# Kernel tuning notes

Measured on AMD Instinct MI355X. Metric: run time of the kernel, lower is better.

The kernel has to match this reference:

```python
import jax, jax.numpy as jnp
import numpy as np

D_MODEL = 1024
NUM_HEADS = 16
D_K = D_MODEL // NUM_HEADS
ROPE_THETA = 10000.0


def _rope(x, positions):
    # x: [B, H, S, Dk]; positions: [S] int. Interleaved-pair RoPE, theta=10000.
    half = D_K // 2
    inv_freq = 1.0 / (ROPE_THETA ** (jnp.arange(half, dtype=jnp.float32) * 2.0 / D_K))
    ang = positions.astype(jnp.float32)[:, None] * inv_freq[None, :]  # [S, half]
    cos = jnp.cos(ang)[None, None]  # [1,1,S,half]
    sin = jnp.sin(ang)[None, None]
    x_even = x[..., 0::2]
    x_odd = x[..., 1::2]
    r_even = x_even * cos - x_odd * sin
    r_odd = x_even * sin + x_odd * cos
    out = jnp.stack([r_even, r_odd], axis=-1)  # [B,H,S,half,2]
    return out.reshape(x.shape)


def setup_inputs() -> dict:
    key = jax.random.key(0)
    ks = jax.random.split(key, 5)
    B, S = 4, 2048
    std = (2.0 / (D_MODEL + D_MODEL)) ** 0.5
    return {
        "x": jax.random.normal(ks[0], (B, S, D_MODEL), dtype=jnp.float32),
        "Wq": jax.random.normal(ks[1], (D_MODEL, D_MODEL), dtype=jnp.float32) * std,
        "Wk": jax.random.normal(ks[2], (D_MODEL, D_MODEL), dtype=jnp.float32) * std,
        "Wv": jax.random.normal(ks[3], (D_MODEL, D_MODEL), dtype=jnp.float32) * std,
        "Wo": jax.random.normal(ks[4], (D_MODEL, D_MODEL), dtype=jnp.float32) * std,
        "token_positions": jnp.arange(S, dtype=jnp.int32),
    }


def reference(x, Wq, Wk, Wv, Wo, token_positions):
    B, S, _ = x.shape
    # QKV projections (weights stored [out, in], y = x @ W^T)
    def proj(W):
        y = jnp.einsum('bsi,oi->bso', x, W)
        return y.reshape(B, S, NUM_HEADS, D_K).transpose(0, 2, 1, 3)  # [B,H,S,Dk]
    q = _rope(proj(Wq), token_positions)
    k = _rope(proj(Wk), token_positions)
    v = proj(Wv)
    scores = jnp.einsum('bhqd,bhkd->bhqk', q, k) / jnp.sqrt(jnp.float32(D_K))
    causal = token_positions[:, None] >= token_positions[None, :]  # [S,S]
    scores = jnp.where(causal[None, None], scores, jnp.float32(-1e9))
    probs = jax.nn.softmax(scores, axis=-1)
    attn = jnp.einsum('bhqk,bhkd->bhqd', probs, v)
    attn = attn.transpose(0, 2, 1, 3).reshape(B, S, D_MODEL)
    return jnp.einsum('bsi,oi->bso', attn, Wo)
```

## Files before the change

kernel.cpp:

```cpp
#include <hip/hip_runtime.h>
#include <hip/hip_bf16.h>
#include <math.h>

#define SEQ 2048
#define BATCH 4
#define MROWS (BATCH*SEQ)
#define DMODEL 1024
#define NHEADS 16
#define DKH 64

typedef float f32x4 __attribute__((ext_vector_type(4)));
typedef float f32x16 __attribute__((ext_vector_type(16)));
typedef __bf16 bf16x8 __attribute__((ext_vector_type(8)));
typedef unsigned short u16;
typedef unsigned int u32;
typedef u16 u16x4 __attribute__((ext_vector_type(4)));
typedef u16 u16x8 __attribute__((ext_vector_type(8)));
typedef u32 u32x4v __attribute__((ext_vector_type(4)));

__device__ __forceinline__ u16 f2bf(float f) {
  union { float f; unsigned u; } v; v.f = f;
  unsigned r = v.u + 0x7FFFu + ((v.u >> 16) & 1u);
  return (u16)(r >> 16);
}

__device__ __forceinline__ void async_copy16(const void* g, void* l) {
  __builtin_amdgcn_global_load_lds(
      (const __attribute__((address_space(1))) void*)g,
      (__attribute__((address_space(3))) void*)l, 16, 0, 0);
}

__device__ __forceinline__ u32 cvtpk(float lo, float hi) {
  u32 r;
  asm("v_cvt_pk_bf16_f32 %0, %1, %2" : "=v"(r) : "v"(lo), "v"(hi));
  return r;
}

__global__ __launch_bounds__(256) void k_prep(
    const float* __restrict__ x,
    const float* __restrict__ Wq, const float* __restrict__ Wk,
    const float* __restrict__ Wv, const float* __restrict__ Wo,
    const int* __restrict__ pos,
    u16* __restrict__ xb, u16* __restrict__ Wqb, u16* __restrict__ Wkb,
    u16* __restrict__ Wvb, u16* __restrict__ Wob,
    float2* __restrict__ csT)
{
  const int bid = blockIdx.x, tid = threadIdx.x;
  if (bid < 8192) {
    int i = bid*256 + tid;
    float4 v = ((const float4*)x)[i];
    u16x4 o; o[0]=f2bf(v.x); o[1]=f2bf(v.y); o[2]=f2bf(v.z); o[3]=f2bf(v.w);
    ((u16x4*)xb)[i] = o;
  } else if (bid < 12288) {
    int wi = (bid - 8192) >> 10;
    const float* src = (wi==0)?Wq:(wi==1)?Wk:(wi==2)?Wv:Wo;
    u16* dst = (wi==0)?Wqb:(wi==1)?Wkb:(wi==2)?Wvb:Wob;
    int i = ((bid - 8192) & 1023)*256 + tid;
    float4 v = ((const float4*)src)[i];
    u16x4 o; o[0]=f2bf(v.x); o[1]=f2bf(v.y); o[2]=f2bf(v.z); o[3]=f2bf(v.w);
    ((u16x4*)dst)[i] = o;
  } else {
    int i = (bid - 12288)*256 + tid;
    int s = i >> 5, j = i & 31;
    float p = (float)pos[s];
    float inv = __builtin_exp2f((float)j * -0.4152410118f);
    float a = p * inv;
    csT[i] = make_float2(__cosf(a), __sinf(a));
  }
}

template<int MODE>
__global__ __launch_bounds__(512, 4) void k_g5(
    const u16* __restrict__ A,
    const u16* __restrict__ W0, const u16* __restrict__ W1,
    const u16* __restrict__ W2,
    u16* __restrict__ Qo, u16* __restrict__ Ko, u16* __restrict__ Vto,
    float* __restrict__ Fo,
    const float2* __restrict__ csT)
{
  __shared__ alignas(16) u16 Asl[128*64];
  __shared__ alignas(16) u16 Bsl[128*64];

  const int bm = blockIdx.x, y = blockIdx.y;
  int proj, bnl;
  const u16* W;
  if constexpr (MODE == 0) {
    proj = y >> 3; bnl = y & 7;
    W = (proj == 0) ? W0 : (proj == 1) ? W1 : W2;
  } else {
    proj = 3; bnl = y; W = W0;
  }

  const int tid = threadIdx.x;
  const int wave = tid >> 6, lane = tid & 63;
  const int lg = lane >> 4, lr = lane & 15;
  const int wm = wave >> 2, wn = wave & 3;

  const u16* Ab = A + (size_t)(bm*128)*DMODEL;
  const u16* Wb = W + (size_t)(bnl*128)*DMODEL;

  f32x4 acc[4][2];
#pragma unroll
  for (int i = 0; i < 4; ++i)
#pragma unroll
    for (int j = 0; j < 2; ++j) acc[i][j] = (f32x4){0,0,0,0};

  for (int t = 0; t < 16; ++t) {
    const int k0 = t * 64;
#pragma unroll
    for (int i = 0; i < 2; ++i) {
      const int idx = i*512 + tid;
      const int row = idx >> 3, ch = idx & 7;
      const int sc = (ch ^ (row & 7)) * 8;
      async_copy16(Ab + (size_t)row*DMODEL + k0 + sc, (char*)Asl + idx*16);
      async_copy16(Wb + (size_t)row*DMODEL + k0 + sc, (char*)Bsl + idx*16);
    }
    __syncthreads();
#pragma unroll
    for (int kk = 0; kk < 2; ++kk) {
      bf16x8 bfr[2];
#pragma unroll
      for (int ni = 0; ni < 2; ++ni) {
        const int row = wn*32 + ni*16 + lr;
        bfr[ni] = *(const bf16x8*)&Bsl[row*64 + (((kk*4 + lg) ^ (row & 7)) * 8)];
      }
#pragma unroll
      for (int mi = 0; mi < 4; ++mi) {
        const int row = wm*64 + mi*16 + lr;
        bf16x8 af = *(const bf16x8*)&Asl[row*64 + (((kk*4 + lg) ^ (row & 7)) * 8)];
#pragma unroll
        for (int ni = 0; ni < 2; ++ni)
          acc[mi][ni] = __builtin_amdgcn_mfma_f32_16x16x32_bf16(af, bfr[ni], acc[mi][ni], 0, 0, 0);
      }
    }
    __syncthreads();
  }

#pragma unroll
  for (int mi = 0; mi < 4; ++mi) {
    const int row0 = bm*128 + wm*64 + mi*16 + lg*4;
#pragma unroll
    for (int ni = 0; ni < 2; ++ni) {
      const int col = bnl*128 + wn*32 + ni*16 + lr;
      f32x4 a = acc[mi][ni];
      if constexpr (MODE == 1) {
#pragma unroll
        for (int r = 0; r < 4; ++r) Fo[(size_t)(row0+r)*DMODEL + col] = a[r];
      } else {
        if (proj == 2) {
          const int hh = col >> 6, dd = col & 63;
          const int s0r = row0 & (SEQ-1);
          const int bb = row0 >> 11;
          u16x4 wv;
#pragma unroll
          for (int r = 0; r < 4; ++r) wv[r] = f2bf(a[r]);
          *(u16x4*)&Vto[((size_t)((bb*16+hh)*64 + dd))*SEQ + s0r] = wv;
        } else {
          u16* C = (proj == 0) ? Qo : Ko;
          const float scl = (proj == 0) ? 0.18033688f : 1.0f;
          const int dd = col & 63;
          const int jj = dd >> 1;
          const float sgn = (dd & 1) ? 1.0f : -1.0f;
#pragma unroll
          for (int r = 0; r < 4; ++r) {
            const int s = (row0 + r) & (SEQ-1);
            float v = a[r];
            float pv = __shfl_xor(v, 1, 64);
            float2 cs = csT[s*32 + jj];
            C[(size_t)(row0+r)*DMODEL + col] = f2bf((v*cs.x + sgn*pv*cs.y) * scl);
          }
        }
      }
    }
  }
}

__global__ __launch_bounds__(512) void k_attn(
    const u16* __restrict__ Q, const u16* __restrict__ K,
    const u16* __restrict__ Vt, u16* __restrict__ O)
{
  const int B = blockIdx.x;
  const int bh = ((B & 7) << 3) | ((B >> 3) & 7);
  const int qt = 7 - (B >> 6);
  const int b = bh >> 4, h = bh & 15;
  const int wave = threadIdx.x >> 6, lane = threadIdx.x & 63;
  const int ql = lane & 31, hi = lane >> 5, hi4 = hi * 4;
  const int R0 = qt*256 + wave*32;

  __shared__ alignas(16) u16 Ks[2][64*64];
  __shared__ alignas(16) u16 Vs[2][64*64];

  const u16* Qb = Q + (size_t)(b*SEQ)*DMODEL + h*64;
  const u16* Kb = K + (size_t)(b*SEQ)*DMODEL + h*64;
  const u16* Vb = Vt + (size_t)(bh*64)*SEQ;

  bf16x8 qf[4];
#pragma unroll
  for (int j = 0; j < 4; ++j)
    qf[j] = *(const bf16x8*)(Qb + (size_t)(R0 + ql)*DMODEL + j*16 + hi*8);

  union { u16x8 u; bf16x8 v; } onesu;
#pragma unroll
  for (int i = 0; i < 8; ++i) onesu.u[i] = 0x3F80;
  const bf16x8 ones = onesu.v;

  f32x16 o0 = (f32x16)(0.f), o1 = (f32x16)(0.f);
  f32x16 lacc = (f32x16)(0.f);
  float m_run = -INFINITY;
  const float THR2 = 11.5415603f;

  const int KT = (qt + 1) * 4;
  const int qp = (ql & ~12) | ((ql & 4) << 1) | ((ql & 8) >> 1);

  auto stage = [&](int buf, int kt) {
    const int idx = threadIdx.x;
    const int row = idx >> 3, ch = idx & 7;
    const int sch = (ch ^ (row & 7)) * 8;
    const int k0 = kt * 64;
    async_copy16(Kb + (size_t)(k0 + row)*DMODEL + sch, (char*)Ks[buf] + idx*16);
    async_copy16(Vb + (size_t)row*SEQ + k0 + sch,      (char*)Vs[buf] + idx*16);
  };

  stage(0, 0);
  __syncthreads();

  for (int kt = 0; kt < KT; ++kt) {
    const int cur = kt & 1;
    if (kt + 1 < KT) stage(cur ^ 1, kt + 1);

    const int k0 = kt*64;
    if (k0 <= R0 + 31) {
      const u16* Kw = Ks[cur];
      const u16* Vw = Vs[cur];

      bf16x8 ka[2][4];
#pragma unroll
      for (int st = 0; st < 2; ++st)
#pragma unroll
        for (int j = 0; j < 4; ++j) {
          const int rk = st*32 + qp;
          const int c = (2*j + hi) ^ (rk & 7);
          ka[st][j] = *(const bf16x8*)&Kw[rk*64 + c*8];
        }
      f32x16 s0 = (f32x16)(0.f), s1 = (f32x16)(0.f);
#pragma unroll
      for (int j = 0; j < 4; ++j) {
        s0 = __builtin_amdgcn_mfma_f32_32x32x16_bf16(ka[0][j], qf[j], s0, 0, 0, 0);
        s1 = __builtin_amdgcn_mfma_f32_32x32x16_bf16(ka[1][j], qf[j], s1, 0, 0, 0);
      }

      if (k0 + 63 > R0) {
        const int base = k0 - R0;
#pragma unroll
        for (int r = 0; r < 16; ++r) {
          const int kl = (r & 7) + (hi << 3) + ((r & 8) << 1);
          s0[r] = (ql >= base + kl)      ? s0[r] : -1e30f;
          s1[r] = (ql >= base + 32 + kl) ? s1[r] : -1e30f;
        }
      }

      float t[16];
#pragma unroll
      for (int r = 0; r < 16; ++r) t[r] = fmaxf(s0[r], s1[r]);
#pragma unroll
      for (int w = 8; w >= 1; w >>= 1)
#pragma unroll
        for (int r = 0; r < w; ++r) t[r] = fmaxf(t[r], t[r+w]);
      const float mx = fmaxf(t[0], __shfl_xor(t[0], 32, 64));

      if (__any(mx > m_run + THR2)) {
        const float mn = fmaxf(m_run, mx);
        const float al = __builtin_exp2f(m_run - mn);
        m_run = mn;
        lacc[0] *= al;
#pragma unroll
        for (int r = 0; r < 16; ++r) { o0[r] *= al; o1[r] *= al; }
      }

      float e0[16], e1[16];
#pragma unroll
      for (int r = 0; r < 16; ++r) {
        e0[r] = __builtin_exp2f(s0[r] - m_run);
        e1[r] = __builtin_exp2f(s1[r] - m_run);
      }

      bf16x8 pb[4];
#pragma unroll
      for (int sl = 0; sl < 4; ++sl) {
        const float* e = (sl < 2) ? e0 : e1;
        const int o8 = (sl & 1) * 8;
        u32 w0 = cvtpk(e[o8+0], e[o8+1]);
        u32 w1 = cvtpk(e[o8+2], e[o8+3]);
        u32 w2 = cvtpk(e[o8+4], e[o8+5]);
        u32 w3 = cvtpk(e[o8+6], e[o8+7]);
        union { u32x4v u; bf16x8 v; } uu;
        uu.u = (u32x4v){w0, w1, w2, w3};
        pb[sl] = uu.v;
      }

#pragma unroll
      for (int sl = 0; sl < 4; ++sl) {
        const int c0 = 2*sl + hi;
        const int d0 = ql,      ca = (c0 ^ (d0 & 7));
        const int d1 = 32 + ql, cb = (c0 ^ (d1 & 7));
        bf16x8 va0 = *(const bf16x8*)&Vw[d0*64 + ca*8];
        bf16x8 va1 = *(const bf16x8*)&Vw[d1*64 + cb*8];
        o0 = __builtin_amdgcn_mfma_f32_32x32x16_bf16(va0, pb[sl], o0, 0, 0, 0);
        o1 = __builtin_amdgcn_mfma_f32_32x32x16_bf16(va1, pb[sl], o1, 0, 0, 0);
        lacc = __builtin_amdgcn_mfma_f32_32x32x16_bf16(ones, pb[sl], lacc, 0, 0, 0);
      }
    }
    __syncthreads();
  }

  const float inv = 1.0f / lacc[0];
  u16* Orow = O + (size_t)(b*SEQ + R0 + ql)*DMODEL + h*64;
#pragma unroll
  for (int rb = 0; rb < 4; ++rb) {
    u16x4 wA, wB;
#pragma unroll
    for (int j = 0; j < 4; ++j) {
      wA[j] = f2bf(o0[rb*4 + j] * inv);
      wB[j] = f2bf(o1[rb*4 + j] * inv);
    }
    *(u16x4*)(Orow + 8*rb + hi4)      = wA;
    *(u16x4*)(Orow + 32 + 8*rb + hi4) = wB;
  }
}

extern "C" void kernel_launch(void* const* d_in, const int* in_sizes, int n_in,
                              void* d_out, int out_size, void* d_ws, size_t ws_size,
                              hipStream_t stream) {
  const float* x  = (const float*)d_in[0];
  const float* Wq = (const float*)d_in[1];
  const float* Wk = (const float*)d_in[2];
  const float* Wv = (const float*)d_in[3];
  const float* Wo = (const float*)d_in[4];
  const int* pos  = (const int*)d_in[5];
  float* out = (float*)d_out;

  const size_t SZ_X   = (size_t)MROWS*DMODEL*2;
  const size_t SZ_W   = (size_t)DMODEL*DMODEL*2;
  const size_t SZ_TAB = (size_t)SEQ*32*8;
  char* w = (char*)d_ws;
  u16* xb   = (u16*)(w);
  u16* Wqb  = (u16*)(w + SZ_X);
  u16* Wkb  = (u16*)(w + SZ_X + SZ_W);
  u16* Wvb  = (u16*)(w + SZ_X + 2*SZ_W);
  u16* Wob  = (u16*)(w + SZ_X + 3*SZ_W);
  float2* csT = (float2*)(w + SZ_X + 4*SZ_W);
  u16* Qb   = (u16*)(w + SZ_X + 4*SZ_W + SZ_TAB);
  u16* Kb   = (u16*)(w + 2*SZ_X + 4*SZ_W + SZ_TAB);
  u16* Ob   = (u16*)(w + 3*SZ_X + 4*SZ_W + SZ_TAB);
  u16* Vt   = (u16*)(w + 4*SZ_X + 4*SZ_W + SZ_TAB);
  const size_t need = 5*SZ_X + 4*SZ_W + SZ_TAB;
  if (ws_size < need) return;

  k_prep<<<12544, 256, 0, stream>>>(x, Wq, Wk, Wv, Wo, pos,
                                    xb, Wqb, Wkb, Wvb, Wob, csT);
  k_g5<0><<<dim3(64, 24), 512, 0, stream>>>(
      xb, Wqb, Wkb, Wvb, Qb, Kb, Vt, nullptr, csT);
  k_attn<<<512, 512, 0, stream>>>(Qb, Kb, Vt, Ob);
  k_g5<1><<<dim3(64, 8), 512, 0, stream>>>(
      Ob, Wob, nullptr, nullptr, nullptr, nullptr, nullptr, out, csT);
}
```

Before: 183.6 us.

## Rework attention kernel: register-staged prefetch, shuffle row sums, new swizzle, setprio

Several changes land together in the attention kernel. The async global-to-LDS copies become register prefetch loads that are written to the other LDS buffer after compute, and the LDS XOR swizzle key now also folds in bit 3 of the row. The row-sum MFMA against a ones vector is replaced by a VALU reduction plus a cross-half shuffle, s_setprio is raised around the MFMA blocks, and the block-to-q-tile order is changed so heavy and light tiles interleave. Together these aim to cut MFMA work, LDS bank conflicts and load-balance tail, at the cost of extra VGPRs for the prefetch registers and more VALU work per tile.

```diff
diff --git a/kernel.cpp b/kernel.cpp
--- a/kernel.cpp
+++ b/kernel.cpp
@@ -17,6 +17,8 @@
 typedef u16 u16x4 __attribute__((ext_vector_type(4)));
 typedef u16 u16x8 __attribute__((ext_vector_type(8)));
 typedef u32 u32x4v __attribute__((ext_vector_type(4)));
+
+#define SWZKEY(r) (((r) & 7) ^ ((((r) >> 3) & 1) << 2))
 
 __device__ __forceinline__ u16 f2bf(float f) {
   union { float f; unsigned u; } v; v.f = f;
@@ -181,7 +183,8 @@
 {
   const int B = blockIdx.x;
   const int bh = ((B & 7) << 3) | ((B >> 3) & 7);
-  const int qt = 7 - (B >> 6);
+  const int g = B >> 6;
+  const int qt = (g < 4) ? (7 - g) : (g - 4);
   const int b = bh >> 4, h = bh & 15;
   const int wave = threadIdx.x >> 6, lane = threadIdx.x & 63;
   const int ql = lane & 31, hi = lane >> 5, hi4 = hi * 4;
@@ -199,34 +202,30 @@
   for (int j = 0; j < 4; ++j)
     qf[j] = *(const bf16x8*)(Qb + (size_t)(R0 + ql)*DMODEL + j*16 + hi*8);
 
-  union { u16x8 u; bf16x8 v; } onesu;
-#pragma unroll
-  for (int i = 0; i < 8; ++i) onesu.u[i] = 0x3F80;
-  const bf16x8 ones = onesu.v;
-
   f32x16 o0 = (f32x16)(0.f), o1 = (f32x16)(0.f);
-  f32x16 lacc = (f32x16)(0.f);
-  float m_run = -INFINITY;
+  float m_run = -INFINITY, l_run = 0.f;
   const float THR2 = 11.5415603f;
 
   const int KT = (qt + 1) * 4;
   const int qp = (ql & ~12) | ((ql & 4) << 1) | ((ql & 8) >> 1);
 
-  auto stage = [&](int buf, int kt) {
-    const int idx = threadIdx.x;
-    const int row = idx >> 3, ch = idx & 7;
-    const int sch = (ch ^ (row & 7)) * 8;
-    const int k0 = kt * 64;
-    async_copy16(Kb + (size_t)(k0 + row)*DMODEL + sch, (char*)Ks[buf] + idx*16);
-    async_copy16(Vb + (size_t)row*SEQ + k0 + sch,      (char*)Vs[buf] + idx*16);
-  };
-
-  stage(0, 0);
+  const int sidx = threadIdx.x;
+  const int srow = sidx >> 3, schk = sidx & 7;
+  const int soff = (schk ^ SWZKEY(srow)) * 8;
+
+  u16x8 kreg = *(const u16x8*)(Kb + (size_t)srow*DMODEL + soff);
+  u16x8 vreg = *(const u16x8*)(Vb + (size_t)srow*SEQ + soff);
+  *(u16x8*)&Ks[0][sidx*8] = kreg;
+  *(u16x8*)&Vs[0][sidx*8] = vreg;
   __syncthreads();
 
   for (int kt = 0; kt < KT; ++kt) {
     const int cur = kt & 1;
-    if (kt + 1 < KT) stage(cur ^ 1, kt + 1);
+    if (kt + 1 < KT) {
+      const int kn = (kt + 1) * 64;
+      kreg = *(const u16x8*)(Kb + (size_t)(kn + srow)*DMODEL + soff);
+      vreg = *(const u16x8*)(Vb + (size_t)srow*SEQ + kn + soff);
+    }
 
     const int k0 = kt*64;
     if (k0 <= R0 + 31) {
@@ -239,15 +238,17 @@
 #pragma unroll
         for (int j = 0; j < 4; ++j) {
           const int rk = st*32 + qp;
-          const int c = (2*j + hi) ^ (rk & 7);
+          const int c = (2*j + hi) ^ SWZKEY(rk);
           ka[st][j] = *(const bf16x8*)&Kw[rk*64 + c*8];
         }
       f32x16 s0 = (f32x16)(0.f), s1 = (f32x16)(0.f);
+      __builtin_amdgcn_s_setprio(1);
 #pragma unroll
       for (int j = 0; j < 4; ++j) {
         s0 = __builtin_amdgcn_mfma_f32_32x32x16_bf16(ka[0][j], qf[j], s0, 0, 0, 0);
         s1 = __builtin_amdgcn_mfma_f32_32x32x16_bf16(ka[1][j], qf[j], s1, 0, 0, 0);
       }
+      __builtin_amdgcn_s_setprio(0);
 
       if (k0 + 63 > R0) {
         const int base = k0 - R0;
@@ -272,7 +273,7 @@
         const float mn = fmaxf(m_run, mx);
         const float al = __builtin_exp2f(m_run - mn);
         m_run = mn;
-        lacc[0] *= al;
+        l_run *= al;
 #pragma unroll
         for (int r = 0; r < 16; ++r) { o0[r] *= al; o1[r] *= al; }
       }
@@ -283,6 +284,13 @@
         e0[r] = __builtin_exp2f(s0[r] - m_run);
         e1[r] = __builtin_exp2f(s1[r] - m_run);
       }
+#pragma unroll
+      for (int r = 0; r < 16; ++r) t[r] = e0[r] + e1[r];
+#pragma unroll
+      for (int w = 8; w >= 1; w >>= 1)
+#pragma unroll
+        for (int r = 0; r < w; ++r) t[r] += t[r+w];
+      l_run += t[0] + __shfl_xor(t[0], 32, 64);
 
       bf16x8 pb[4];
 #pragma unroll
@@ -298,22 +306,28 @@
         pb[sl] = uu.v;
       }
 
+      __builtin_amdgcn_s_setprio(1);
 #pragma unroll
       for (int sl = 0; sl < 4; ++sl) {
         const int c0 = 2*sl + hi;
-        const int d0 = ql,      ca = (c0 ^ (d0 & 7));
-        const int d1 = 32 + ql, cb = (c0 ^ (d1 & 7));
+        const int d0 = ql,      ca = (c0 ^ SWZKEY(d0));
+        const int d1 = 32 + ql, cb = (c0 ^ SWZKEY(d1));
         bf16x8 va0 = *(const bf16x8*)&Vw[d0*64 + ca*8];
         bf16x8 va1 = *(const bf16x8*)&Vw[d1*64 + cb*8];
         o0 = __builtin_amdgcn_mfma_f32_32x32x16_bf16(va0, pb[sl], o0, 0, 0, 0);
         o1 = __builtin_amdgcn_mfma_f32_32x32x16_bf16(va1, pb[sl], o1, 0, 0, 0);
-        lacc = __builtin_amdgcn_mfma_f32_32x32x16_bf16(ones, pb[sl], lacc, 0, 0, 0);
-      }
+      }
+      __builtin_amdgcn_s_setprio(0);
+    }
+
+    if (kt + 1 < KT) {
+      *(u16x8*)&Ks[cur ^ 1][sidx*8] = kreg;
+      *(u16x8*)&Vs[cur ^ 1][sidx*8] = vreg;
     }
     __syncthreads();
   }
 
-  const float inv = 1.0f / lacc[0];
+  const float inv = 1.0f / l_run;
   u16* Orow = O + (size_t)(b*SEQ + R0 + ql)*DMODEL + h*64;
 #pragma unroll
   for (int rb = 0; rb < 4; ++rb) {
```

After: 192.8 us. 1.05x slower.
